# Kernel optimization log

Hardware: AMD Instinct MI355X
Metric: run time of the kernel (lower is better)

## Reference

```python
import jax, jax.numpy as jnp
import numpy as np

CAPACITY = 0.125


def setup_inputs() -> dict:
    key = jax.random.key(0)
    ks = jax.random.split(key, 6)
    b, s, d, dff = 4, 8192, 512, 2048
    x = jax.random.normal(ks[0], (b, s, d), dtype=jnp.float32)
    position_ids = jnp.tile(jnp.arange(s, dtype=jnp.int64)[None, :], (b, 1))
    Wr = jax.random.normal(ks[1], (d,), dtype=jnp.float32) * 0.02
    br = jnp.zeros((1,), dtype=jnp.float32)
    W1 = jax.random.normal(ks[2], (d, dff), dtype=jnp.float32) * 0.02
    b1 = jnp.zeros((dff,), dtype=jnp.float32)
    W2 = jax.random.normal(ks[3], (dff, d), dtype=jnp.float32) * 0.02
    b2 = jnp.zeros((d,), dtype=jnp.float32)
    return {"x": x, "position_ids": position_ids, "Wr": Wr, "br": br,
            "W1": W1, "b1": b1, "W2": W2, "b2": b2}


def reference(x, position_ids, Wr, br, W1, b1, W2, b2):
    b, s, d = x.shape
    # Router: Linear(d, 1) -> squeeze(-1)
    weights = jnp.einsum('bsd,d->bs', x, Wr) + br  # [b, s]
    k = int(CAPACITY * s)
    # Per-batch top-k threshold (k-th largest value)
    top_k_values = jax.lax.top_k(weights, k)[0]  # [b, k], sorted desc
    threshold = top_k_values[:, -1]              # [b]
    selected_mask = weights > threshold[:, None]  # strict >, ties excluded (matches torch)
    # Block: per-token MLP (Linear-GELU-Linear). Per-token ops commute with the
    # gather/scatter, so computing densely and masking is mathematically identical
    # to the original gather -> block -> weighted scatter.
    h = jax.nn.gelu(jnp.einsum('bsd,df->bsf', x, W1) + b1)
    y = jnp.einsum('bsf,fd->bsd', h, W2) + b2
    # processed_tokens (= block_out * router_weight on selected) + x on unselected
    out = jnp.where(selected_mask[..., None], y * weights[..., None], x)
    return out
```

## Files before the change

kernel.cpp:

```cpp
#include <hip/hip_runtime.h>
#include <hip/hip_bf16.h>

#define B_   4
#define S_   8192
#define D_   512
#define DFF_ 2048
#define K_TOP 1024

typedef unsigned short u16;
typedef __attribute__((ext_vector_type(8))) short bf16x8;
typedef __attribute__((ext_vector_type(4))) float floatx4;

__device__ __forceinline__ unsigned f2key(float f){
    unsigned u = __float_as_uint(f);
    return (u & 0x80000000u) ? ~u : (u | 0x80000000u);
}
__device__ __forceinline__ u16 f2b(float f){
    unsigned u = __float_as_uint(f);
    u = (u + 0x7FFFu + ((u >> 16) & 1u)) >> 16;
    return (u16)u;
}
__device__ __forceinline__ float gelu_fast(float v){
    float u = 1.5957691216f * v + 0.0713548162726f * v * v * v;
    float e = __expf(u);
    return v - v / (e + 1.0f);
}
__device__ __forceinline__ void gl_lds16(const void* gptr, void* lptr){
    auto g = (const __attribute__((address_space(1))) unsigned int*)((uintptr_t)gptr);
    auto l = (__attribute__((address_space(3))) unsigned int*)((uintptr_t)lptr);
    __builtin_amdgcn_global_load_lds(g, l, 16, 0, 0);
}


__global__ __launch_bounds__(256) void prep_kernel(
    const float* __restrict__ W1, const float* __restrict__ W2,
    u16* __restrict__ W1t, u16* __restrict__ W2t,
    const float4* __restrict__ x,
    const float4* __restrict__ Wr4, const float* __restrict__ br,
    float* __restrict__ w_all, unsigned* __restrict__ ghist)
{
    __shared__ __align__(16) unsigned char shmem[128 * 132 * 2];
    const int tid = threadIdx.x;
    const int bx = blockIdx.x;
    if (bx < 128){
        const float* src; u16* dst; int R, C, ct, ks;
        if (bx < 64){ src = W1; dst = W1t; R = D_;   C = DFF_; ct = bx & 15;        ks = bx >> 4; }
        else        { src = W2; dst = W2t; R = DFF_; C = D_;   ct = (bx - 64) & 3;  ks = (bx - 64) >> 2; }
        u16 (*tile)[132] = (u16(*)[132])shmem;
        #pragma unroll
        for (int it = 0; it < 64; it++){
            int lin = it * 256 + tid;
            int kk = lin >> 7, nn = lin & 127;
            tile[kk][nn] = f2b(src[(size_t)(ks * 128 + kk) * C + ct * 128 + nn]);
        }
        __syncthreads();
        u16* base = dst + (size_t)(ct * (R / 128) + ks) * 16384;
        const int r = tid >> 1, h = tid & 1;
        #pragma unroll
        for (int c = 0; c < 8; c++){
            int cl = h * 8 + c;
            bf16x8 bv;
            #pragma unroll
            for (int e = 0; e < 8; e++) bv[e] = (short)tile[cl * 8 + e][r];
            *(bf16x8*)&base[r * 128 + ((cl ^ (r & 15)) << 3)] = bv;
        }
    } else {
        unsigned* hist = (unsigned*)shmem;
        if (tid < 256) hist[tid] = 0u;
        __syncthreads();
        const int wb = bx - 128;
        const int wv = tid >> 6, lane = tid & 63;
        const int t0 = wb * 64 + wv * 16;
        const float brv = br[0];
        const float4 wr0 = Wr4[lane], wr1 = Wr4[lane + 64];
        #pragma unroll
        for (int g = 0; g < 4; g++){
            float a[4];
            #pragma unroll
            for (int tt = 0; tt < 4; tt++){
                const float4* xt = x + (size_t)(t0 + g * 4 + tt) * 128;
                float4 v0 = xt[lane], v1 = xt[lane + 64];
                a[tt] = v0.x*wr0.x + v0.y*wr0.y + v0.z*wr0.z + v0.w*wr0.w
                      + v1.x*wr1.x + v1.y*wr1.y + v1.z*wr1.z + v1.w*wr1.w;
            }
            #pragma unroll
            for (int off = 32; off > 0; off >>= 1){
                #pragma unroll
                for (int tt = 0; tt < 4; tt++) a[tt] += __shfl_down(a[tt], off, 64);
            }
            if (lane == 0){
                #pragma unroll
                for (int tt = 0; tt < 4; tt++){
                    float wt = a[tt] + brv;
                    w_all[t0 + g * 4 + tt] = wt;
                    atomicAdd(&hist[f2key(wt) >> 24], 1u);
                }
            }
        }
        __syncthreads();
        if (tid < 256) ghist[wb * 256 + tid] = hist[tid];
    }
}

__global__ __launch_bounds__(1024) void kth_compact_kernel(
    const float4* __restrict__ w_all4, const unsigned* __restrict__ ghist,
    int* __restrict__ counts, unsigned* __restrict__ thr_out,
    int* __restrict__ idx)
{
    __shared__ unsigned keys[S_];
    __shared__ unsigned hist[4][256];
    __shared__ unsigned sprefix;
    __shared__ int sremk;
    __shared__ int lbase;
    const int b = blockIdx.x, tid = threadIdx.x;
    const int wv = tid >> 6, lane = tid & 63;
    const float4* row4 = w_all4 + (size_t)b * (S_ / 4);

    #pragma unroll
    for (int i = 0; i < 2; i++){
        int j = tid + i * 1024;
        float4 v = row4[j];
        keys[4*j+0] = f2key(v.x); keys[4*j+1] = f2key(v.y);
        keys[4*j+2] = f2key(v.z); keys[4*j+3] = f2key(v.w);
    }
    {
        const int bin = tid & 255, q = tid >> 8;
        unsigned s = 0;
        const unsigned* gh = ghist + (size_t)(b * 128 + q * 32) * 256 + bin;
        #pragma unroll 8
        for (int j = 0; j < 32; j++) s += gh[j * 256];
        hist[q][bin] = s;
    }
    if (tid == 0){ sprefix = 0u; sremk = K_TOP; lbase = 0; }
    __syncthreads();

    for (int pass = 3; pass >= 0; pass--){
        const int shift = pass * 8;
        if (pass < 3){
            ((unsigned*)hist)[tid] = 0u;
            __syncthreads();
            const unsigned mask_hi = 0xFFFFFFFFu << (shift + 8);
            const unsigned pfx = sprefix;
            #pragma unroll
            for (int i = 0; i < 8; i++){
                unsigned key = keys[tid + i * 1024];
                if ((key & mask_hi) == pfx)
                    atomicAdd(&hist[wv & 3][(key >> shift) & 255u], 1u);
            }
            __syncthreads();
        }
        if (wv == 0){
            const unsigned remk = (unsigned)sremk;
            const unsigned pfx = sprefix;
            unsigned c[4];
            #pragma unroll
            for (int q = 0; q < 4; q++)
                c[q] = hist[0][4*lane+q] + hist[1][4*lane+q]
                     + hist[2][4*lane+q] + hist[3][4*lane+q];
            unsigned t = c[0] + c[1] + c[2] + c[3];
            unsigned ss = t;
            #pragma unroll
            for (int off = 1; off < 64; off <<= 1){
                unsigned o = __shfl_down(ss, off, 64);
                ss += (lane + off < 64) ? o : 0u;
            }
            const unsigned sgt = ss - t;
            unsigned suf[4];
            suf[3] = c[3] + sgt; suf[2] = c[2] + suf[3];
            suf[1] = c[1] + suf[2]; suf[0] = c[0] + suf[1];
            #pragma unroll
            for (int q = 0; q < 4; q++){
                unsigned nx = suf[q] - c[q];
                if (suf[q] >= remk && nx < remk){
                    sprefix = pfx | ((unsigned)(4 * lane + q) << shift);
                    sremk = (int)(remk - nx);
                }
            }
        }
        __syncthreads();
    }

    const unsigned thr = sprefix;
    #pragma unroll
    for (int i = 0; i < 8; i++){
        int li = tid + i * 1024;
        bool sel = keys[li] > thr;
        unsigned long long m = __ballot(sel);
        int wtot = (int)__popcll(m);
        if (wtot){
            int woff = 0;
            if (lane == 0) woff = atomicAdd(&lbase, wtot);
            woff = __shfl(woff, 0, 64);
            if (sel){
                int pos = woff + (int)__popcll(m & ((1ull << lane) - 1ull));
                idx[b * 1024 + pos] = b * S_ + li;
            }
        }
    }
    __syncthreads();
    if (tid == 0){ counts[b] = lbase; thr_out[b] = thr; }
}

__global__ __launch_bounds__(256) void gather_kernel(
    const float* __restrict__ x, const int* __restrict__ idx,
    const int* __restrict__ counts, u16* __restrict__ XbT)
{
    const int mt = blockIdx.x, s = blockIdx.y;
    const int cl = threadIdx.x & 15, r16 = threadIdx.x >> 4;
    u16* base = XbT + (size_t)(mt * 4 + s) * 16384;
    #pragma unroll
    for (int it = 0; it < 8; it++){
        int r = r16 + it * 16;
        int mg = mt * 128 + r;
        if ((mg & 1023) < counts[mg >> 10]){
            const float* xp = x + (size_t)idx[mg] * D_ + s * 128 + cl * 8;
            float4 v0 = *(const float4*)xp;
            float4 v1 = *(const float4*)(xp + 4);
            bf16x8 bv;
            bv[0]=(short)f2b(v0.x); bv[1]=(short)f2b(v0.y);
            bv[2]=(short)f2b(v0.z); bv[3]=(short)f2b(v0.w);
            bv[4]=(short)f2b(v1.x); bv[5]=(short)f2b(v1.y);
            bv[6]=(short)f2b(v1.z); bv[7]=(short)f2b(v1.w);
            *(bf16x8*)&base[r * 128 + ((cl ^ (r & 15)) << 3)] = bv;
        }
    }
}

__device__ __forceinline__ void tail_copy(
    const float4* __restrict__ x, float4* __restrict__ out,
    const float* __restrict__ w_all, const unsigned* __restrict__ thr,
    int tBase, int perWave, int tid)
{
    const int wv = tid >> 6, lane = tid & 63;
    const int t0 = tBase + wv * perWave;
    for (int tt = 0; tt < perWave; tt++){
        int t = t0 + tt;
        if (f2key(w_all[t]) <= thr[t >> 13]){
            const float4* xs = x + (size_t)t * 128;
            float4* od = out + (size_t)t * 128;
            od[lane]      = xs[lane];
            od[lane + 64] = xs[lane + 64];
        }
    }
}

__global__ __launch_bounds__(256) void ffn1_kernel(
    const u16* __restrict__ XbT, const u16* __restrict__ W1t,
    const int* __restrict__ counts, const float* __restrict__ bias1,
    u16* __restrict__ Ht,
    const float4* __restrict__ x, float4* __restrict__ out,
    const float* __restrict__ w_all, const unsigned* __restrict__ thr)
{
    __shared__ __align__(16) u16 smem[32768];
    const int tid = threadIdx.x;
    const int bx = blockIdx.x;
    const int mBlk = bx & 31, nBlk = bx >> 5;
    const int lane = tid & 63, w = tid >> 6;
    const int wr = (w >> 1) * 64, wc = (w & 1) * 64;
    const int fr = lane & 15, quad = lane >> 4;

    const char* Abase = (const char*)(XbT + (size_t)mBlk * 4 * 16384);
    const char* Bbase = (const char*)(W1t + (size_t)nBlk * 4 * 16384);
    char* Al0 = (char*)smem + tid * 16;
    char* Bl0 = (char*)(smem + 16384) + tid * 16;
    const int rr0 = tid >> 3, pp = tid & 7;

    auto stage = [&](const char* gbase, char* lb, int hs){
        const char* s0 = gbase + (size_t)(hs >> 1) * 32768;
        const int h = hs & 1;
        #pragma unroll
        for (int i = 0; i < 4; i++){
            int r = rr0 + i * 32;
            int pg = pp | (((h ^ (r >> 3)) & 1) << 3);
            gl_lds16(s0 + r * 256 + pg * 16, lb + i * 4096);
        }
    };

    stage(Abase, Al0, 0);
    stage(Bbase, Bl0, 0);

    floatx4 acc[4][4] = {};
    for (int hs = 0; hs < 8; hs++){
        __builtin_amdgcn_s_barrier();
        if (hs + 1 < 8){
            stage(Abase, Al0 + ((hs + 1) & 1) * 16384, hs + 1);
            stage(Bbase, Bl0 + ((hs + 1) & 1) * 16384, hs + 1);
            asm volatile("s_waitcnt vmcnt(8)" ::: "memory");
        } else {
            asm volatile("s_waitcnt vmcnt(0)" ::: "memory");
        }
        __builtin_amdgcn_sched_barrier(0);
        __builtin_amdgcn_s_barrier();
        const u16* Ab = smem + (hs & 1) * 8192;
        const u16* Bb = smem + 16384 + (hs & 1) * 8192;
        __builtin_amdgcn_s_setprio(1);
        #pragma unroll
        for (int ks2 = 0; ks2 < 2; ks2++){
            bf16x8 af[4], bf[4];
            #pragma unroll
            for (int i = 0; i < 4; i++){
                int r = wr + i * 16 + fr;
                af[i] = *(const bf16x8*)&Ab[r * 64 + (((ks2 * 4 + quad) ^ (r & 7)) << 3)];
            }
            #pragma unroll
            for (int j = 0; j < 4; j++){
                int r = wc + j * 16 + fr;
                bf[j] = *(const bf16x8*)&Bb[r * 64 + (((ks2 * 4 + quad) ^ (r & 7)) << 3)];
            }
            #pragma unroll
            for (int i = 0; i < 4; i++)
                #pragma unroll
                for (int j = 0; j < 4; j++)
                    acc[i][j] = __builtin_amdgcn_mfma_f32_16x16x32_bf16(af[i], bf[j], acc[i][j], 0, 0, 0);
        }
        __builtin_amdgcn_s_setprio(0);
    }

    float bj[4];
    #pragma unroll
    for (int j = 0; j < 4; j++) bj[j] = bias1[nBlk * 128 + wc + j * 16 + fr];

    __syncthreads();
    u16* Cs = smem;
    #pragma unroll
    for (int i = 0; i < 4; i++){
        #pragma unroll
        for (int rg = 0; rg < 4; rg++){
            int r = wr + i * 16 + quad * 4 + rg;
            #pragma unroll
            for (int j = 0; j < 4; j++){
                int col = wc + j * 16 + fr;
                float v = gelu_fast(acc[i][j][rg] + bj[j]);
                Cs[r * 128 + ((((col >> 3) ^ (r & 15)) << 3) | (col & 7))] = f2b(v);
            }
        }
    }
    __syncthreads();
    const int r = tid >> 1, h = tid & 1;
    int mg = mBlk * 128 + r;
    if ((mg & 1023) < counts[mg >> 10]){
        u16* dstp = Ht + (((size_t)(mBlk * 2 + (r >> 6)) * 16 + nBlk) * 64 + (r & 63)) * 128;
        #pragma unroll
        for (int p = 0; p < 8; p++){
            int pc = h * 8 + p;
            *(bf16x8*)&dstp[pc << 3] = *(const bf16x8*)&Cs[r * 128 + (pc << 3)];
        }
    }
    tail_copy(x, out, w_all, thr, bx * 32, 8, tid);
}

__global__ __launch_bounds__(256) void ffn2_kernel(
    const u16* __restrict__ Ht, const u16* __restrict__ W2t,
    const int* __restrict__ counts, const int* __restrict__ idx,
    const float* __restrict__ w_all, const float* __restrict__ bias2,
    float* __restrict__ out,
    const float4* __restrict__ x, const unsigned* __restrict__ thr)
{
    __shared__ __align__(16) u16 smem[24576];
    const int tid = threadIdx.x;
    const int bx = blockIdx.x;
    const int mBlk = bx & 63, nBlk = bx >> 6;
    const int lane = tid & 63, w = tid >> 6;
    const int wr = (w >> 1) * 32, wc = (w & 1) * 64;
    const int fr = lane & 15, quad = lane >> 4;

    const char* Abase = (const char*)(Ht + (size_t)mBlk * 16 * 8192);
    const char* Bbase = (const char*)(W2t + (size_t)nBlk * 16 * 16384);
    char* Al0 = (char*)smem + tid * 16;
    char* Bl0 = (char*)(smem + 8192) + tid * 16;
    const int rr0 = tid >> 3, pp = tid & 7;

    auto stage = [&](int buf, int hs){
        const int h = hs & 1;
        {
            const char* s0 = Abase + (size_t)(hs >> 1) * 16384;
            char* l = Al0 + buf * 8192;
            #pragma unroll
            for (int i = 0; i < 2; i++){
                int r = rr0 + i * 32;
                int pg = pp | (((h ^ (r >> 3)) & 1) << 3);
                gl_lds16(s0 + r * 256 + pg * 16, l + i * 4096);
            }
        }
        {
            const char* s0 = Bbase + (size_t)(hs >> 1) * 32768;
            char* l = Bl0 + buf * 16384;
            #pragma unroll
            for (int i = 0; i < 4; i++){
                int r = rr0 + i * 32;
                int pg = pp | (((h ^ (r >> 3)) & 1) << 3);
                gl_lds16(s0 + r * 256 + pg * 16, l + i * 4096);
            }
        }
    };

    stage(0, 0);
    floatx4 acc[2][4] = {};
    for (int hs = 0; hs < 32; hs++){
        __builtin_amdgcn_s_barrier();
        if (hs + 1 < 32){
            stage((hs + 1) & 1, hs + 1);
            asm volatile("s_waitcnt vmcnt(6)" ::: "memory");
        } else {
            asm volatile("s_waitcnt vmcnt(0)" ::: "memory");
        }
        __builtin_amdgcn_sched_barrier(0);
        __builtin_amdgcn_s_barrier();
        const u16* Ab = smem + (hs & 1) * 4096;
        const u16* Bb = smem + 8192 + (hs & 1) * 8192;
        __builtin_amdgcn_s_setprio(1);
        #pragma unroll
        for (int ks2 = 0; ks2 < 2; ks2++){
            bf16x8 af[2], bf[4];
            #pragma unroll
            for (int i = 0; i < 2; i++){
                int r = wr + i * 16 + fr;
                af[i] = *(const bf16x8*)&Ab[r * 64 + (((ks2 * 4 + quad) ^ (r & 7)) << 3)];
            }
            #pragma unroll
            for (int j = 0; j < 4; j++){
                int r = wc + j * 16 + fr;
                bf[j] = *(const bf16x8*)&Bb[r * 64 + (((ks2 * 4 + quad) ^ (r & 7)) << 3)];
            }
            #pragma unroll
            for (int i = 0; i < 2; i++)
                #pragma unroll
                for (int j = 0; j < 4; j++)
                    acc[i][j] = __builtin_amdgcn_mfma_f32_16x16x32_bf16(af[i], bf[j], acc[i][j], 0, 0, 0);
        }
        __builtin_amdgcn_s_setprio(0);
    }

    float bj[4];
    #pragma unroll
    for (int j = 0; j < 4; j++) bj[j] = bias2[nBlk * 128 + wc + j * 16 + fr];

    __syncthreads();
    float* Cs = (float*)smem;
    #pragma unroll
    for (int i = 0; i < 2; i++){
        #pragma unroll
        for (int rg = 0; rg < 4; rg++){
            int r = wr + i * 16 + quad * 4 + rg;
            #pragma unroll
            for (int j = 0; j < 4; j++)
                Cs[r * 128 + wc + j * 16 + fr] = acc[i][j][rg] + bj[j];
        }
    }
    __syncthreads();
    const int r = tid >> 2, q = tid & 3;
    int mg = mBlk * 64 + r;
    if ((mg & 1023) < counts[mg >> 10]){
        int token = idx[mg];
        float wt = w_all[token];
        float* op = out + (size_t)token * D_ + nBlk * 128 + q * 32;
        const float4* cp = (const float4*)&Cs[r * 128 + q * 32];
        #pragma unroll
        for (int p = 0; p < 8; p++){
            float4 vv = cp[p];
            vv.x *= wt; vv.y *= wt; vv.z *= wt; vv.w *= wt;
            ((float4*)op)[p] = vv;
        }
    }
    tail_copy(x, (float4*)out, w_all, thr, 16384 + bx * 64, 16, tid);
}

extern "C" void kernel_launch(void* const* d_in, const int* in_sizes, int n_in,
                              void* d_out, int out_size, void* d_ws, size_t ws_size,
                              hipStream_t stream)
{
    const float* x  = (const float*)d_in[0];
    const float* Wr = (const float*)d_in[2];
    const float* br = (const float*)d_in[3];
    const float* W1 = (const float*)d_in[4];
    const float* b1 = (const float*)d_in[5];
    const float* W2 = (const float*)d_in[6];
    const float* b2 = (const float*)d_in[7];
    float* out = (float*)d_out;
    char* ws = (char*)d_ws;

    float*    w_all  = (float*)   (ws + 0);
    int*      counts = (int*)     (ws + 131072);
    unsigned* thr    = (unsigned*)(ws + 131088);
    int*      idx    = (int*)     (ws + 131136);
    unsigned* ghist  = (unsigned*)(ws + 163840);
    u16*      XbT    = (u16*)     (ws + 720896);
    u16*      W1t    = (u16*)     (ws + 4915200);
    u16*      W2t    = (u16*)     (ws + 7012352);
    u16*      Ht     = (u16*)     (ws + 9109504);

    prep_kernel<<<640, 256, 0, stream>>>(
        W1, W2, W1t, W2t, (const float4*)x,
        (const float4*)Wr, br, w_all, ghist);
    kth_compact_kernel<<<B_, 1024, 0, stream>>>(
        (const float4*)w_all, ghist, counts, thr, idx);
    gather_kernel<<<dim3(32, 4), 256, 0, stream>>>(x, idx, counts, XbT);
    ffn1_kernel<<<512, 256, 0, stream>>>(
        XbT, W1t, counts, b1, Ht, (const float4*)x, (float4*)out, w_all, thr);
    ffn2_kernel<<<256, 256, 0, stream>>>(
        Ht, W2t, counts, idx, w_all, b2, out, (const float4*)x, thr);
}
```

Measured before the change: 195.4 us.

## Fuse token gather into FFN1 and copy all of x unconditionally in extra blocks

Removes the separate gather kernel: FFN1 now loads selected token rows of x directly into registers, converts them to bf16 and writes them into LDS per K-step, while W1 tiles are still prefetched asynchronously. The masked tail copy is replaced by extra blocks that copy all of x to out unconditionally, and FFN2 then overwrites the selected rows. This drops a kernel launch, the XbT round trip and the threshold checks. In exchange it adds register staging in the GEMM loop, a full copy of x, and a write-after-write ordering dependency between FFN1's copy and FFN2's scatter, which relies on stream ordering.

```diff
diff --git a/kernel.cpp b/kernel.cpp
--- a/kernel.cpp
+++ b/kernel.cpp
@@ -104,8 +104,7 @@
 
 __global__ __launch_bounds__(1024) void kth_compact_kernel(
     const float4* __restrict__ w_all4, const unsigned* __restrict__ ghist,
-    int* __restrict__ counts, unsigned* __restrict__ thr_out,
-    int* __restrict__ idx)
+    int* __restrict__ counts, int* __restrict__ idx)
 {
     __shared__ unsigned keys[S_];
     __shared__ unsigned hist[4][256];
@@ -198,114 +197,108 @@
         }
     }
     __syncthreads();
-    if (tid == 0){ counts[b] = lbase; thr_out[b] = thr; }
-}
-
-__global__ __launch_bounds__(256) void gather_kernel(
+    if (tid == 0) counts[b] = lbase;
+}
+
+__global__ __launch_bounds__(256) void ffn1_kernel(
     const float* __restrict__ x, const int* __restrict__ idx,
-    const int* __restrict__ counts, u16* __restrict__ XbT)
+    const u16* __restrict__ W1t, const int* __restrict__ counts,
+    const float* __restrict__ bias1, u16* __restrict__ Ht,
+    float4* __restrict__ out)
 {
-    const int mt = blockIdx.x, s = blockIdx.y;
-    const int cl = threadIdx.x & 15, r16 = threadIdx.x >> 4;
-    u16* base = XbT + (size_t)(mt * 4 + s) * 16384;
-    #pragma unroll
-    for (int it = 0; it < 8; it++){
-        int r = r16 + it * 16;
-        int mg = mt * 128 + r;
-        if ((mg & 1023) < counts[mg >> 10]){
-            const float* xp = x + (size_t)idx[mg] * D_ + s * 128 + cl * 8;
-            float4 v0 = *(const float4*)xp;
-            float4 v1 = *(const float4*)(xp + 4);
+    __shared__ __align__(16) u16 smem[24576];
+    const int tid = threadIdx.x, bx = blockIdx.x;
+
+    if (bx >= 512){
+        const int wv = tid >> 6, lane = tid & 63;
+        const int t0 = (bx - 512) * 128 + wv * 32;
+        const float4* x4 = (const float4*)x;
+        for (int tt = 0; tt < 32; tt++){
+            const float4* xs = x4 + (size_t)(t0 + tt) * 128;
+            float4* od = out + (size_t)(t0 + tt) * 128;
+            od[lane]      = xs[lane];
+            od[lane + 64] = xs[lane + 64];
+        }
+        return;
+    }
+
+    const int mBlk = (bx & 7) * 4 + ((bx >> 3) & 3);
+    const int nBlk = bx >> 5;
+    const int lane = tid & 63, w = tid >> 6;
+    const int wr = (w >> 1) * 64, wc = (w & 1) * 64;
+    const int fr = lane & 15, quad = lane >> 4;
+
+    const int r = tid >> 1, h = tid & 1;
+    const int mg = mBlk * 128 + r;
+    const bool valid = (mg & 1023) < counts[mg >> 10];
+    const int tok = valid ? idx[mg] : 0;
+    const float* arow = x + (size_t)tok * 512 + h * 32;
+    u16* Arow = smem + r * 64;
+    const int slotbase = h * 4;
+
+    const char* Bbase = (const char*)(W1t + (size_t)nBlk * 4 * 16384);
+    char* Bl0 = (char*)(smem + 8192) + tid * 16;
+    const int rr0 = tid >> 3, pp = tid & 7;
+    auto stageB = [&](int buf, int hs){
+        const char* s0 = Bbase + (size_t)(hs >> 1) * 32768;
+        const int hh = hs & 1;
+        char* lb = Bl0 + buf * 16384;
+        #pragma unroll
+        for (int i = 0; i < 4; i++){
+            int rb = rr0 + i * 32;
+            int pg = pp | (((hh ^ (rb >> 3)) & 1) << 3);
+            gl_lds16(s0 + rb * 256 + pg * 16, lb + i * 4096);
+        }
+    };
+
+    float4 ra[8];
+    #pragma unroll
+    for (int e = 0; e < 8; e++) ra[e] = ((const float4*)arow)[e];
+    __builtin_amdgcn_sched_barrier(0);
+    stageB(0, 0);
+
+    floatx4 acc[4][4] = {};
+    for (int hs = 0; hs < 8; hs++){
+        __builtin_amdgcn_s_barrier();
+        asm volatile("s_waitcnt vmcnt(4)" ::: "memory");
+        __builtin_amdgcn_sched_barrier(0);
+        #pragma unroll
+        for (int cc = 0; cc < 4; cc++){
+            float4 v0 = ra[cc*2], v1 = ra[cc*2+1];
             bf16x8 bv;
             bv[0]=(short)f2b(v0.x); bv[1]=(short)f2b(v0.y);
             bv[2]=(short)f2b(v0.z); bv[3]=(short)f2b(v0.w);
             bv[4]=(short)f2b(v1.x); bv[5]=(short)f2b(v1.y);
             bv[6]=(short)f2b(v1.z); bv[7]=(short)f2b(v1.w);
-            *(bf16x8*)&base[r * 128 + ((cl ^ (r & 15)) << 3)] = bv;
-        }
-    }
-}
-
-__device__ __forceinline__ void tail_copy(
-    const float4* __restrict__ x, float4* __restrict__ out,
-    const float* __restrict__ w_all, const unsigned* __restrict__ thr,
-    int tBase, int perWave, int tid)
-{
-    const int wv = tid >> 6, lane = tid & 63;
-    const int t0 = tBase + wv * perWave;
-    for (int tt = 0; tt < perWave; tt++){
-        int t = t0 + tt;
-        if (f2key(w_all[t]) <= thr[t >> 13]){
-            const float4* xs = x + (size_t)t * 128;
-            float4* od = out + (size_t)t * 128;
-            od[lane]      = xs[lane];
-            od[lane + 64] = xs[lane + 64];
-        }
-    }
-}
-
-__global__ __launch_bounds__(256) void ffn1_kernel(
-    const u16* __restrict__ XbT, const u16* __restrict__ W1t,
-    const int* __restrict__ counts, const float* __restrict__ bias1,
-    u16* __restrict__ Ht,
-    const float4* __restrict__ x, float4* __restrict__ out,
-    const float* __restrict__ w_all, const unsigned* __restrict__ thr)
-{
-    __shared__ __align__(16) u16 smem[32768];
-    const int tid = threadIdx.x;
-    const int bx = blockIdx.x;
-    const int mBlk = bx & 31, nBlk = bx >> 5;
-    const int lane = tid & 63, w = tid >> 6;
-    const int wr = (w >> 1) * 64, wc = (w & 1) * 64;
-    const int fr = lane & 15, quad = lane >> 4;
-
-    const char* Abase = (const char*)(XbT + (size_t)mBlk * 4 * 16384);
-    const char* Bbase = (const char*)(W1t + (size_t)nBlk * 4 * 16384);
-    char* Al0 = (char*)smem + tid * 16;
-    char* Bl0 = (char*)(smem + 16384) + tid * 16;
-    const int rr0 = tid >> 3, pp = tid & 7;
-
-    auto stage = [&](const char* gbase, char* lb, int hs){
-        const char* s0 = gbase + (size_t)(hs >> 1) * 32768;
-        const int h = hs & 1;
-        #pragma unroll
-        for (int i = 0; i < 4; i++){
-            int r = rr0 + i * 32;
-            int pg = pp | (((h ^ (r >> 3)) & 1) << 3);
-            gl_lds16(s0 + r * 256 + pg * 16, lb + i * 4096);
-        }
-    };
-
-    stage(Abase, Al0, 0);
-    stage(Bbase, Bl0, 0);
-
-    floatx4 acc[4][4] = {};
-    for (int hs = 0; hs < 8; hs++){
-        __builtin_amdgcn_s_barrier();
+            *(bf16x8*)&Arow[(((slotbase + cc) ^ (r & 7)) << 3)] = bv;
+        }
         if (hs + 1 < 8){
-            stage(Abase, Al0 + ((hs + 1) & 1) * 16384, hs + 1);
-            stage(Bbase, Bl0 + ((hs + 1) & 1) * 16384, hs + 1);
-            asm volatile("s_waitcnt vmcnt(8)" ::: "memory");
+            const float4* an = (const float4*)(arow + (hs + 1) * 64);
+            #pragma unroll
+            for (int e = 0; e < 8; e++) ra[e] = an[e];
+            __builtin_amdgcn_sched_barrier(0);
+            stageB((hs + 1) & 1, hs + 1);
+            asm volatile("s_waitcnt vmcnt(12) lgkmcnt(0)" ::: "memory");
         } else {
-            asm volatile("s_waitcnt vmcnt(0)" ::: "memory");
+            asm volatile("s_waitcnt vmcnt(0) lgkmcnt(0)" ::: "memory");
         }
         __builtin_amdgcn_sched_barrier(0);
         __builtin_amdgcn_s_barrier();
-        const u16* Ab = smem + (hs & 1) * 8192;
-        const u16* Bb = smem + 16384 + (hs & 1) * 8192;
+        const u16* Ab = smem;
+        const u16* Bb = (const u16*)((const char*)smem + 16384 + (hs & 1) * 16384);
         __builtin_amdgcn_s_setprio(1);
         #pragma unroll
         for (int ks2 = 0; ks2 < 2; ks2++){
             bf16x8 af[4], bf[4];
             #pragma unroll
             for (int i = 0; i < 4; i++){
-                int r = wr + i * 16 + fr;
-                af[i] = *(const bf16x8*)&Ab[r * 64 + (((ks2 * 4 + quad) ^ (r & 7)) << 3)];
+                int rr = wr + i * 16 + fr;
+                af[i] = *(const bf16x8*)&Ab[rr * 64 + (((ks2 * 4 + quad) ^ (rr & 7)) << 3)];
             }
             #pragma unroll
             for (int j = 0; j < 4; j++){
-                int r = wc + j * 16 + fr;
-                bf[j] = *(const bf16x8*)&Bb[r * 64 + (((ks2 * 4 + quad) ^ (r & 7)) << 3)];
+                int rr = wc + j * 16 + fr;
+                bf[j] = *(const bf16x8*)&Bb[rr * 64 + (((ks2 * 4 + quad) ^ (rr & 7)) << 3)];
             }
             #pragma unroll
             for (int i = 0; i < 4; i++)
@@ -326,35 +319,33 @@
     for (int i = 0; i < 4; i++){
         #pragma unroll
         for (int rg = 0; rg < 4; rg++){
-            int r = wr + i * 16 + quad * 4 + rg;
+            int rr = wr + i * 16 + quad * 4 + rg;
             #pragma unroll
             for (int j = 0; j < 4; j++){
                 int col = wc + j * 16 + fr;
                 float v = gelu_fast(acc[i][j][rg] + bj[j]);
-                Cs[r * 128 + ((((col >> 3) ^ (r & 15)) << 3) | (col & 7))] = f2b(v);
-            }
-        }
-    }
-    __syncthreads();
-    const int r = tid >> 1, h = tid & 1;
-    int mg = mBlk * 128 + r;
-    if ((mg & 1023) < counts[mg >> 10]){
-        u16* dstp = Ht + (((size_t)(mBlk * 2 + (r >> 6)) * 16 + nBlk) * 64 + (r & 63)) * 128;
+                Cs[rr * 128 + ((((col >> 3) ^ (rr & 15)) << 3) | (col & 7))] = f2b(v);
+            }
+        }
+    }
+    __syncthreads();
+    const int cr = tid >> 1, ch = tid & 1;
+    int cmg = mBlk * 128 + cr;
+    if ((cmg & 1023) < counts[cmg >> 10]){
+        u16* dstp = Ht + (((size_t)(mBlk * 2 + (cr >> 6)) * 16 + nBlk) * 64 + (cr & 63)) * 128;
         #pragma unroll
         for (int p = 0; p < 8; p++){
-            int pc = h * 8 + p;
-            *(bf16x8*)&dstp[pc << 3] = *(const bf16x8*)&Cs[r * 128 + (pc << 3)];
-        }
-    }
-    tail_copy(x, out, w_all, thr, bx * 32, 8, tid);
+            int pc = ch * 8 + p;
+            *(bf16x8*)&dstp[pc << 3] = *(const bf16x8*)&Cs[cr * 128 + (pc << 3)];
+        }
+    }
 }
 
 __global__ __launch_bounds__(256) void ffn2_kernel(
     const u16* __restrict__ Ht, const u16* __restrict__ W2t,
     const int* __restrict__ counts, const int* __restrict__ idx,
     const float* __restrict__ w_all, const float* __restrict__ bias2,
-    float* __restrict__ out,
-    const float4* __restrict__ x, const unsigned* __restrict__ thr)
+    float* __restrict__ out)
 {
     __shared__ __align__(16) u16 smem[24576];
     const int tid = threadIdx.x;
@@ -406,8 +397,8 @@
         }
         __builtin_amdgcn_sched_barrier(0);
         __builtin_amdgcn_s_barrier();
-        const u16* Ab = smem + (hs & 1) * 4096;
-        const u16* Bb = smem + 8192 + (hs & 1) * 8192;
+        const u16* Ab = (const u16*)((const char*)smem + (hs & 1) * 8192);
+        const u16* Bb = (const u16*)((const char*)smem + 16384 + (hs & 1) * 16384);
         __builtin_amdgcn_s_setprio(1);
         #pragma unroll
         for (int ks2 = 0; ks2 < 2; ks2++){
@@ -462,7 +453,6 @@
             ((float4*)op)[p] = vv;
         }
     }
-    tail_copy(x, (float4*)out, w_all, thr, 16384 + bx * 64, 16, tid);
 }
 
 extern "C" void kernel_launch(void* const* d_in, const int* in_sizes, int n_in,
@@ -481,10 +471,8 @@
 
     float*    w_all  = (float*)   (ws + 0);
     int*      counts = (int*)     (ws + 131072);
-    unsigned* thr    = (unsigned*)(ws + 131088);
     int*      idx    = (int*)     (ws + 131136);
     unsigned* ghist  = (unsigned*)(ws + 163840);
-    u16*      XbT    = (u16*)     (ws + 720896);
     u16*      W1t    = (u16*)     (ws + 4915200);
     u16*      W2t    = (u16*)     (ws + 7012352);
     u16*      Ht     = (u16*)     (ws + 9109504);
@@ -493,10 +481,9 @@
         W1, W2, W1t, W2t, (const float4*)x,
         (const float4*)Wr, br, w_all, ghist);
     kth_compact_kernel<<<B_, 1024, 0, stream>>>(
-        (const float4*)w_all, ghist, counts, thr, idx);
-    gather_kernel<<<dim3(32, 4), 256, 0, stream>>>(x, idx, counts, XbT);
-    ffn1_kernel<<<512, 256, 0, stream>>>(
-        XbT, W1t, counts, b1, Ht, (const float4*)x, (float4*)out, w_all, thr);
+        (const float4*)w_all, ghist, counts, idx);
+    ffn1_kernel<<<768, 256, 0, stream>>>(
+        x, idx, W1t, counts, b1, Ht, (float4*)out);
     ffn2_kernel<<<256, 256, 0, stream>>>(
-        Ht, W2t, counts, idx, w_all, b2, out, (const float4*)x, thr);
-}
+        Ht, W2t, counts, idx, w_all, b2, out);
+}
```

After: 196.0 us. About the same (+0.3%).

## Fuse passthrough copy of x into router prep pass and swizzle FFN1 block order

Applied to the files above, without the earlier changes.

The router prep pass already reads every x row, so it now writes that row straight to out as well. The per-token tail_copy in both FFN kernels is removed, along with the threshold buffer it used; ffn2 later overwrites the selected rows. This removes a second full read of x and the per-token threshold checks, at the cost of also writing the selected rows that get overwritten later. The copy traffic moves into the serial prep stage, where it no longer overlaps the GEMMs. FFN1 also remaps its M-block index from the block id, likely to improve L2 reuse of weight tiles across concurrent blocks.

```diff
diff --git a/kernel.cpp b/kernel.cpp
--- a/kernel.cpp
+++ b/kernel.cpp
@@ -35,7 +35,7 @@
 __global__ __launch_bounds__(256) void prep_kernel(
     const float* __restrict__ W1, const float* __restrict__ W2,
     u16* __restrict__ W1t, u16* __restrict__ W2t,
-    const float4* __restrict__ x,
+    const float4* __restrict__ x, float4* __restrict__ out,
     const float4* __restrict__ Wr4, const float* __restrict__ br,
     float* __restrict__ w_all, unsigned* __restrict__ ghist)
 {
@@ -78,8 +78,11 @@
             float a[4];
             #pragma unroll
             for (int tt = 0; tt < 4; tt++){
-                const float4* xt = x + (size_t)(t0 + g * 4 + tt) * 128;
+                const int t = t0 + g * 4 + tt;
+                const float4* xt = x + (size_t)t * 128;
+                float4* ot = out + (size_t)t * 128;
                 float4 v0 = xt[lane], v1 = xt[lane + 64];
+                ot[lane] = v0; ot[lane + 64] = v1;
                 a[tt] = v0.x*wr0.x + v0.y*wr0.y + v0.z*wr0.z + v0.w*wr0.w
                       + v1.x*wr1.x + v1.y*wr1.y + v1.z*wr1.z + v1.w*wr1.w;
             }
@@ -104,8 +107,7 @@
 
 __global__ __launch_bounds__(1024) void kth_compact_kernel(
     const float4* __restrict__ w_all4, const unsigned* __restrict__ ghist,
-    int* __restrict__ counts, unsigned* __restrict__ thr_out,
-    int* __restrict__ idx)
+    int* __restrict__ counts, int* __restrict__ idx)
 {
     __shared__ unsigned keys[S_];
     __shared__ unsigned hist[4][256];
@@ -198,7 +200,7 @@
         }
     }
     __syncthreads();
-    if (tid == 0){ counts[b] = lbase; thr_out[b] = thr; }
+    if (tid == 0) counts[b] = lbase;
 }
 
 __global__ __launch_bounds__(256) void gather_kernel(
@@ -226,35 +228,15 @@
     }
 }
 
-__device__ __forceinline__ void tail_copy(
-    const float4* __restrict__ x, float4* __restrict__ out,
-    const float* __restrict__ w_all, const unsigned* __restrict__ thr,
-    int tBase, int perWave, int tid)
-{
-    const int wv = tid >> 6, lane = tid & 63;
-    const int t0 = tBase + wv * perWave;
-    for (int tt = 0; tt < perWave; tt++){
-        int t = t0 + tt;
-        if (f2key(w_all[t]) <= thr[t >> 13]){
-            const float4* xs = x + (size_t)t * 128;
-            float4* od = out + (size_t)t * 128;
-            od[lane]      = xs[lane];
-            od[lane + 64] = xs[lane + 64];
-        }
-    }
-}
-
 __global__ __launch_bounds__(256) void ffn1_kernel(
     const u16* __restrict__ XbT, const u16* __restrict__ W1t,
     const int* __restrict__ counts, const float* __restrict__ bias1,
-    u16* __restrict__ Ht,
-    const float4* __restrict__ x, float4* __restrict__ out,
-    const float* __restrict__ w_all, const unsigned* __restrict__ thr)
+    u16* __restrict__ Ht)
 {
     __shared__ __align__(16) u16 smem[32768];
-    const int tid = threadIdx.x;
-    const int bx = blockIdx.x;
-    const int mBlk = bx & 31, nBlk = bx >> 5;
+    const int tid = threadIdx.x, bx = blockIdx.x;
+    const int mBlk = (bx & 7) * 4 + ((bx >> 3) & 3);
+    const int nBlk = bx >> 5;
     const int lane = tid & 63, w = tid >> 6;
     const int wr = (w >> 1) * 64, wc = (w & 1) * 64;
     const int fr = lane & 15, quad = lane >> 4;
@@ -346,15 +328,13 @@
             *(bf16x8*)&dstp[pc << 3] = *(const bf16x8*)&Cs[r * 128 + (pc << 3)];
         }
     }
-    tail_copy(x, out, w_all, thr, bx * 32, 8, tid);
 }
 
 __global__ __launch_bounds__(256) void ffn2_kernel(
     const u16* __restrict__ Ht, const u16* __restrict__ W2t,
     const int* __restrict__ counts, const int* __restrict__ idx,
     const float* __restrict__ w_all, const float* __restrict__ bias2,
-    float* __restrict__ out,
-    const float4* __restrict__ x, const unsigned* __restrict__ thr)
+    float* __restrict__ out)
 {
     __shared__ __align__(16) u16 smem[24576];
     const int tid = threadIdx.x;
@@ -406,8 +386,8 @@
         }
         __builtin_amdgcn_sched_barrier(0);
         __builtin_amdgcn_s_barrier();
-        const u16* Ab = smem + (hs & 1) * 4096;
-        const u16* Bb = smem + 8192 + (hs & 1) * 8192;
+        const u16* Ab = (const u16*)((const char*)smem + (hs & 1) * 8192);
+        const u16* Bb = (const u16*)((const char*)smem + 16384 + (hs & 1) * 16384);
         __builtin_amdgcn_s_setprio(1);
         #pragma unroll
         for (int ks2 = 0; ks2 < 2; ks2++){
@@ -462,7 +442,6 @@
             ((float4*)op)[p] = vv;
         }
     }
-    tail_copy(x, (float4*)out, w_all, thr, 16384 + bx * 64, 16, tid);
 }
 
 extern "C" void kernel_launch(void* const* d_in, const int* in_sizes, int n_in,
@@ -481,7 +460,6 @@
 
     float*    w_all  = (float*)   (ws + 0);
     int*      counts = (int*)     (ws + 131072);
-    unsigned* thr    = (unsigned*)(ws + 131088);
     int*      idx    = (int*)     (ws + 131136);
     unsigned* ghist  = (unsigned*)(ws + 163840);
     u16*      XbT    = (u16*)     (ws + 720896);
@@ -490,13 +468,13 @@
     u16*      Ht     = (u16*)     (ws + 9109504);
 
     prep_kernel<<<640, 256, 0, stream>>>(
-        W1, W2, W1t, W2t, (const float4*)x,
+        W1, W2, W1t, W2t, (const float4*)x, (float4*)out,
         (const float4*)Wr, br, w_all, ghist);
     kth_compact_kernel<<<B_, 1024, 0, stream>>>(
-        (const float4*)w_all, ghist, counts, thr, idx);
+        (const float4*)w_all, ghist, counts, idx);
     gather_kernel<<<dim3(32, 4), 256, 0, stream>>>(x, idx, counts, XbT);
     ffn1_kernel<<<512, 256, 0, stream>>>(
-        XbT, W1t, counts, b1, Ht, (const float4*)x, (float4*)out, w_all, thr);
+        XbT, W1t, counts, b1, Ht);
     ffn2_kernel<<<256, 256, 0, stream>>>(
-        Ht, W2t, counts, idx, w_all, b2, out, (const float4*)x, thr);
-}
+        Ht, W2t, counts, idx, w_all, b2, out);
+}
```

Measured after the change: 186.7 us. 1.05x faster.
